# Optimization experiments

Hardware: AMD Instinct MI355X
Metric: run time of the kernel (lower is better)

The kernel has to match this reference:

```python
import jax, jax.numpy as jnp
import numpy as np

N_VIS, N_ASSOC, N_MOTOR, IN_DIM, T = 8192, 4096, 1024, 4096, 16
TAU_MEM, V_TH, TAU_ELIG = 20.0, 1.0, 500.0


def setup_inputs() -> dict:
    key = jax.random.key(0)
    ks = jax.random.split(key, 8)
    visual_input = jax.random.uniform(ks[0], (T, IN_DIM), dtype=jnp.float32)
    noise = jax.random.uniform(ks[1], (T, N_VIS), dtype=jnp.float32)  # replaces torch.rand_like
    dopamine = jax.random.normal(ks[2], (T,), dtype=jnp.float32)
    # visual_encoder: nn.Linear(4096, n_visual) default init (kaiming-uniform-ish); use small uniform
    lim = 1.0 / np.sqrt(IN_DIM)
    W_enc = jax.random.uniform(ks[3], (N_VIS, IN_DIM), minval=-lim, maxval=lim, dtype=jnp.float32)
    b_enc = jax.random.uniform(ks[4], (N_VIS,), minval=-lim, maxval=lim, dtype=jnp.float32)
    # v_to_a / a_to_m: uniform_(0.01, 0.05), no bias
    W_va = jax.random.uniform(ks[5], (N_ASSOC, N_VIS), minval=0.01, maxval=0.05, dtype=jnp.float32)
    W_am = jax.random.uniform(ks[6], (N_MOTOR, N_ASSOC), minval=0.01, maxval=0.05, dtype=jnp.float32)
    return {"visual_input": visual_input, "noise": noise, "dopamine": dopamine,
            "W_enc": W_enc, "b_enc": b_enc, "W_va": W_va, "W_am": W_am}


def reference(visual_input, noise, dopamine, W_enc, b_enc, W_va, W_am):
    decay_m = 1.0 - 1.0 / TAU_MEM
    decay_e = 1.0 - 1.0 / TAU_ELIG
    f32 = jnp.float32

    def step(carry, xs):
        vV, vA, vM, eVA, eAM, Wva, Wam = carry
        x, u, d = xs
        # visual encoding + Bernoulli spikes
        rates = jax.nn.sigmoid(x @ W_enc.T + b_enc)             # [n_visual]
        in_spk = (u < rates * 0.3).astype(f32)
        # LIF: visual layer
        vV = vV * decay_m + in_spk
        v_spk = (vV > V_TH).astype(f32)
        vV = vV * (1.0 - v_spk)
        # LIF: assoc layer
        vA = vA * decay_m + (v_spk @ Wva.T) * 0.1
        a_spk = (vA > V_TH).astype(f32)
        vA = vA * (1.0 - a_spk)
        # LIF: motor layer
        vM = vM * decay_m + (a_spk @ Wam.T) * 0.1
        m_spk = (vM > V_TH).astype(f32)
        vM = vM * (1.0 - m_spk)
        # DA-STDP eligibility traces (rank-1 updates)
        eVA = eVA * decay_e + jnp.outer(v_spk, a_spk) * 0.01    # [n_visual, n_assoc]
        eAM = eAM * decay_e + jnp.outer(a_spk, m_spk) * 0.01    # [n_assoc, n_motor]
        # conditional dopamine-gated weight update
        gate = jnp.abs(d) > 0.1
        Wva_new = jnp.clip(Wva + jnp.clip(d * eVA.T * 0.1, -0.01, 0.01), 0.0, 1.0)
        Wam_new = jnp.clip(Wam + jnp.clip(d * eAM.T * 0.1, -0.01, 0.01), 0.0, 1.0)
        Wva = jnp.where(gate, Wva_new, Wva)
        Wam = jnp.where(gate, Wam_new, Wam)
        eVA = jnp.where(gate, eVA * 0.5, eVA)
        eAM = jnp.where(gate, eAM * 0.5, eAM)
        return (vV, vA, vM, eVA, eAM, Wva, Wam), m_spk

    init = (jnp.zeros(N_VIS, f32), jnp.zeros(N_ASSOC, f32), jnp.zeros(N_MOTOR, f32),
            jnp.zeros((N_VIS, N_ASSOC), f32), jnp.zeros((N_ASSOC, N_MOTOR), f32),
            W_va, W_am)
    _, motor_spikes = jax.lax.scan(step, init, (visual_input, noise, dopamine))
    return motor_spikes  # [T, n_motor]
```

## Files before the change

### kernel.cpp

```cpp
#include <hip/hip_runtime.h>
#include <cstdint>

#define N_VIS   8192
#define N_ASSOC 4096
#define N_MOTOR 1024
#define IN_DIM  4096
#define T_STEPS 16

__global__ __launch_bounds__(256, 4) void encoder_kernel(
        const float* __restrict__ x, const float* __restrict__ noise,
        const float* __restrict__ W, const float* __restrict__ b,
        unsigned* __restrict__ vmask) {
    __shared__ float4 xs[16 * 64];
    const int tid = threadIdx.x;
    const int wave = tid >> 6, lane = tid & 63;
    const int r0 = blockIdx.x * 8 + wave * 2;
    const float4* W0 = (const float4*)(W + (size_t)r0 * IN_DIM);
    const float4* W1 = (const float4*)(W + (size_t)(r0 + 1) * IN_DIM);

    float a0[T_STEPS], a1[T_STEPS];
#pragma unroll
    for (int t = 0; t < T_STEPS; ++t) { a0[t] = 0.f; a1[t] = 0.f; }

    for (int c = 0; c < 16; ++c) {
        __syncthreads();
#pragma unroll
        for (int p = 0; p < 4; ++p) {
            int f = tid + p * 256;
            int t = f >> 6, c4 = f & 63;
            xs[f] = ((const float4*)(x + (size_t)t * IN_DIM + c * 256))[c4];
        }
        __syncthreads();
        float4 w0 = W0[c * 64 + lane];
        float4 w1 = W1[c * 64 + lane];
#pragma unroll
        for (int t = 0; t < T_STEPS; ++t) {
            float4 xv = xs[t * 64 + lane];
            a0[t] += w0.x*xv.x + w0.y*xv.y + w0.z*xv.z + w0.w*xv.w;
            a1[t] += w1.x*xv.x + w1.y*xv.y + w1.z*xv.z + w1.w*xv.w;
        }
    }
#pragma unroll
    for (int t = 0; t < T_STEPS; ++t) {
        float v;
        v = a0[t]; for (int o = 32; o; o >>= 1) v += __shfl_xor(v, o, 64); a0[t] = v;
        v = a1[t]; for (int o = 32; o; o >>= 1) v += __shfl_xor(v, o, 64); a1[t] = v;
    }
    if (lane == 0) {
        auto do_row = [&](int i, const float (&a)[T_STEPS]) {
            float bb = b[i];
            float v = 0.f;
            unsigned msk = 0;
#pragma unroll
            for (int t = 0; t < T_STEPS; ++t) {
                float logit = a[t] + bb;
                float rate = 1.0f / (1.0f + expf(-logit));
                float u = noise[t * N_VIS + i];
                float ins = (u < rate * 0.3f) ? 1.0f : 0.0f;
                v = v * 0.95f + ins;
                if (v > 1.0f) { msk |= (1u << t); v = 0.f; }
            }
            vmask[i] = msk;
        };
        do_row(r0, a0);
        do_row(r0 + 1, a1);
    }
}

__global__ void ktab_kernel(const float* __restrict__ dop, float* __restrict__ K) {
    __shared__ float C[256];
    __shared__ float sd[16];
    __shared__ unsigned sg[16];
    const int p = threadIdx.x;
    if (p < 16) {
        float d = dop[p];
        sd[p] = d;
        sg[p] = (fabsf(d) > 0.1f) ? 1u : 0u;
    }
    __syncthreads();
    {
        const int s = p >> 4, r = p & 15;
        float c = 0.f;
        if (s >= r) {
            c = 1.f;
            for (int u = r; u < s; ++u) {
                if (sg[u]) c *= 0.5f;
                c *= 0.998f;
            }
        }
        C[p] = c;
    }
    __syncthreads();
    {
        const int t = p >> 4, r = p & 15;
        float kk = 0.f;
        for (int s = r; s < t; ++s)
            if (sg[s]) kk += ((sd[s] * 0.1f) * 0.01f) * C[s * 16 + r];
        K[p] = kk;
    }
}

__global__ void ovl_kernel(const unsigned* __restrict__ mask, int words_per_block,
                           int* __restrict__ ovl) {
    const int p = threadIdx.x;
    const int r = p >> 4, t = p & 15;
    const unsigned* w = mask + blockIdx.x * words_per_block;
    int c = 0;
    for (int i = 0; i < words_per_block; ++i)
        c += (int)((w[i] >> r) & (w[i] >> t) & 1u);
    atomicAdd(&ovl[p], c);
}

template<int NC>
__global__ __launch_bounds__(256) void base_kernel(
        const float* __restrict__ W0, const unsigned* __restrict__ colmask,
        float* __restrict__ base) {
    const int j0 = blockIdx.x * 2;
    const int tid = threadIdx.x;
    const int lane = tid & 63, wv = tid >> 6;
    __shared__ float sred[4][32];

    const float4* Wr0 = (const float4*)(W0 + (size_t)j0 * (NC * 1024));
    const float4* Wr1 = (const float4*)(W0 + (size_t)(j0 + 1) * (NC * 1024));
    const uint4*  cm  = (const uint4*)colmask;

    float acc0[T_STEPS], acc1[T_STEPS];
#pragma unroll
    for (int t = 0; t < T_STEPS; ++t) { acc0[t] = 0.f; acc1[t] = 0.f; }

    for (int k = 0; k < NC; ++k) {
        float4 q0 = Wr0[tid + k * 256];
        float4 q1 = Wr1[tid + k * 256];
        uint4  m  = cm [tid + k * 256];
        unsigned plo = m.x | (m.y << 16);
        unsigned phi = m.z | (m.w << 16);
#pragma unroll
        for (int t = 0; t < T_STEPS; ++t) {
            float bx = (float)((plo >> t)        & 1u);
            float by = (float)((plo >> (t + 16)) & 1u);
            float bz = (float)((phi >> t)        & 1u);
            float bw = (float)((phi >> (t + 16)) & 1u);
            acc0[t] = fmaf(q0.x, bx, acc0[t]); acc0[t] = fmaf(q0.y, by, acc0[t]);
            acc0[t] = fmaf(q0.z, bz, acc0[t]); acc0[t] = fmaf(q0.w, bw, acc0[t]);
            acc1[t] = fmaf(q1.x, bx, acc1[t]); acc1[t] = fmaf(q1.y, by, acc1[t]);
            acc1[t] = fmaf(q1.z, bz, acc1[t]); acc1[t] = fmaf(q1.w, bw, acc1[t]);
        }
    }
#pragma unroll
    for (int t = 0; t < T_STEPS; ++t) {
        for (int o = 32; o; o >>= 1) acc0[t] += __shfl_down(acc0[t], o, 64);
        for (int o = 32; o; o >>= 1) acc1[t] += __shfl_down(acc1[t], o, 64);
    }
    if (lane == 0) {
#pragma unroll
        for (int t = 0; t < T_STEPS; ++t) {
            sred[wv][t]      = acc0[t];
            sred[wv][16 + t] = acc1[t];
        }
    }
    __syncthreads();
    if (tid < 32) {
        const int r = tid >> 4, t = tid & 15;
        float v = sred[0][tid] + sred[1][tid] + sred[2][tid] + sred[3][tid];
        base[(size_t)(j0 + r) * 16 + t] = v;
    }
}

__global__ __launch_bounds__(64) void rec_kernel(
        const float* __restrict__ base, const int* __restrict__ ovl,
        const float* __restrict__ K, unsigned* __restrict__ mask_out,
        float* __restrict__ outp, int out_stride) {
    __shared__ float KO[256];
    const int tid = threadIdx.x;
    for (int p = tid; p < 256; p += 64) {
        const int t = p >> 4, r = p & 15;
        KO[p] = K[p] * (float)ovl[r * 16 + t];
    }
    __syncthreads();

    const int j = blockIdx.x * 64 + tid;
    float br[T_STEPS];
#pragma unroll
    for (int t = 0; t < T_STEPS; ++t) br[t] = base[(size_t)j * 16 + t];

    float vmem = 0.f;
    unsigned am = 0;
#pragma unroll
    for (int t = 0; t < T_STEPS; ++t) {
        float I = br[t];
        for (int r = 0; r < t; ++r)
            if ((am >> r) & 1u) I += KO[t * 16 + r];
        vmem = vmem * 0.95f + I * 0.1f;
        const bool s = vmem > 1.0f;
        if (s) { vmem = 0.f; am |= (1u << t); }
        if (outp) outp[t * out_stride + j] = s ? 1.0f : 0.0f;
    }
    mask_out[j] = am;
}

extern "C" void kernel_launch(void* const* d_in, const int* in_sizes, int n_in,
                              void* d_out, int out_size, void* d_ws, size_t ws_size,
                              hipStream_t stream) {
    const float* x     = (const float*)d_in[0];
    const float* noise = (const float*)d_in[1];
    const float* dop   = (const float*)d_in[2];
    const float* W_enc = (const float*)d_in[3];
    const float* b_enc = (const float*)d_in[4];
    const float* W_va  = (const float*)d_in[5];
    const float* W_am  = (const float*)d_in[6];
    float* out = (float*)d_out;
    (void)in_sizes; (void)n_in; (void)out_size; (void)ws_size;

    char* ws = (char*)d_ws;
    size_t off = 0;
    unsigned* vmask  = (unsigned*)(ws + off); off += N_VIS * 4;
    unsigned* amask  = (unsigned*)(ws + off); off += N_ASSOC * 4;
    unsigned* mmask  = (unsigned*)(ws + off); off += N_MOTOR * 4;
    float*    K      = (float*)(ws + off);    off += 256 * 4;
    int*      ovl_v  = (int*)(ws + off);      off += 256 * 4;
    int*      ovl_a  = (int*)(ws + off);      off += 256 * 4;
    float*    baseVA = (float*)(ws + off);    off += (size_t)N_ASSOC * 16 * 4;
    float*    baseAM = (float*)(ws + off);    off += (size_t)N_MOTOR * 16 * 4;

    hipMemsetAsync(ovl_v, 0, 2 * 256 * 4, stream);

    ktab_kernel<<<1, 256, 0, stream>>>(dop, K);
    encoder_kernel<<<N_VIS / 8, 256, 0, stream>>>(x, noise, W_enc, b_enc, vmask);
    ovl_kernel<<<32, 256, 0, stream>>>(vmask, N_VIS / 32, ovl_v);
    base_kernel<8><<<N_ASSOC / 2, 256, 0, stream>>>(W_va, vmask, baseVA);
    rec_kernel<<<N_ASSOC / 64, 64, 0, stream>>>(baseVA, ovl_v, K, amask, nullptr, 0);
    ovl_kernel<<<16, 256, 0, stream>>>(amask, N_ASSOC / 16, ovl_a);
    base_kernel<4><<<N_MOTOR / 2, 256, 0, stream>>>(W_am, amask, baseAM);
    rec_kernel<<<N_MOTOR / 64, 64, 0, stream>>>(baseAM, ovl_a, K, mmask, out, N_MOTOR);
}
```

Before: 158.0 us.

## Double-buffer encoder input tiles and assign one row per wave in encoder and base kernels

```diff
diff --git a/kernel.cpp b/kernel.cpp
--- a/kernel.cpp
+++ b/kernel.cpp
@@ -7,63 +7,67 @@
 #define IN_DIM  4096
 #define T_STEPS 16
 
-__global__ __launch_bounds__(256, 4) void encoder_kernel(
+__global__ __launch_bounds__(512, 8) void encoder_kernel(
         const float* __restrict__ x, const float* __restrict__ noise,
         const float* __restrict__ W, const float* __restrict__ b,
         unsigned* __restrict__ vmask) {
-    __shared__ float4 xs[16 * 64];
+    __shared__ float4 xs[2][16 * 64];
     const int tid = threadIdx.x;
     const int wave = tid >> 6, lane = tid & 63;
-    const int r0 = blockIdx.x * 8 + wave * 2;
-    const float4* W0 = (const float4*)(W + (size_t)r0 * IN_DIM);
-    const float4* W1 = (const float4*)(W + (size_t)(r0 + 1) * IN_DIM);
-
-    float a0[T_STEPS], a1[T_STEPS];
-#pragma unroll
-    for (int t = 0; t < T_STEPS; ++t) { a0[t] = 0.f; a1[t] = 0.f; }
-
+    const int r = blockIdx.x * 8 + wave;
+    const float4* Wr = (const float4*)(W + (size_t)r * IN_DIM);
+
+    float a[T_STEPS];
+#pragma unroll
+    for (int t = 0; t < T_STEPS; ++t) a[t] = 0.f;
+
+    auto stage = [&](int c, int buf) {
+#pragma unroll
+        for (int p = 0; p < 2; ++p) {
+            int f = tid + p * 512;
+            int t = f >> 6, c4 = f & 63;
+            xs[buf][f] = ((const float4*)(x + (size_t)t * IN_DIM + c * 256))[c4];
+        }
+    };
+    stage(0, 0);
+    float4 wv = Wr[lane];
+    __syncthreads();
+
+#pragma unroll 1
     for (int c = 0; c < 16; ++c) {
+        const int cb = c & 1;
+        if (c < 15) stage(c + 1, cb ^ 1);
+        float4 nwv = wv;
+        if (c < 15) nwv = Wr[(c + 1) * 64 + lane];
+#pragma unroll
+        for (int t = 0; t < T_STEPS; ++t) {
+            float4 xv = xs[cb][t * 64 + lane];
+            a[t] += wv.x*xv.x + wv.y*xv.y + wv.z*xv.z + wv.w*xv.w;
+        }
         __syncthreads();
-#pragma unroll
-        for (int p = 0; p < 4; ++p) {
-            int f = tid + p * 256;
-            int t = f >> 6, c4 = f & 63;
-            xs[f] = ((const float4*)(x + (size_t)t * IN_DIM + c * 256))[c4];
-        }
-        __syncthreads();
-        float4 w0 = W0[c * 64 + lane];
-        float4 w1 = W1[c * 64 + lane];
+        wv = nwv;
+    }
+
+#pragma unroll
+    for (int t = 0; t < T_STEPS; ++t) {
+        float v = a[t];
+        for (int o = 32; o; o >>= 1) v += __shfl_xor(v, o, 64);
+        a[t] = v;
+    }
+    if (lane == 0) {
+        float bb = b[r];
+        float v = 0.f;
+        unsigned msk = 0;
 #pragma unroll
         for (int t = 0; t < T_STEPS; ++t) {
-            float4 xv = xs[t * 64 + lane];
-            a0[t] += w0.x*xv.x + w0.y*xv.y + w0.z*xv.z + w0.w*xv.w;
-            a1[t] += w1.x*xv.x + w1.y*xv.y + w1.z*xv.z + w1.w*xv.w;
-        }
-    }
-#pragma unroll
-    for (int t = 0; t < T_STEPS; ++t) {
-        float v;
-        v = a0[t]; for (int o = 32; o; o >>= 1) v += __shfl_xor(v, o, 64); a0[t] = v;
-        v = a1[t]; for (int o = 32; o; o >>= 1) v += __shfl_xor(v, o, 64); a1[t] = v;
-    }
-    if (lane == 0) {
-        auto do_row = [&](int i, const float (&a)[T_STEPS]) {
-            float bb = b[i];
-            float v = 0.f;
-            unsigned msk = 0;
-#pragma unroll
-            for (int t = 0; t < T_STEPS; ++t) {
-                float logit = a[t] + bb;
-                float rate = 1.0f / (1.0f + expf(-logit));
-                float u = noise[t * N_VIS + i];
-                float ins = (u < rate * 0.3f) ? 1.0f : 0.0f;
-                v = v * 0.95f + ins;
-                if (v > 1.0f) { msk |= (1u << t); v = 0.f; }
-            }
-            vmask[i] = msk;
-        };
-        do_row(r0, a0);
-        do_row(r0 + 1, a1);
+            float logit = a[t] + bb;
+            float rate = 1.0f / (1.0f + expf(-logit));
+            float u = noise[t * N_VIS + r];
+            float ins = (u < rate * 0.3f) ? 1.0f : 0.0f;
+            v = v * 0.95f + ins;
+            if (v > 1.0f) { msk |= (1u << t); v = 0.f; }
+        }
+        vmask[r] = msk;
     }
 }
 
@@ -112,57 +116,46 @@
 }
 
 template<int NC>
-__global__ __launch_bounds__(256) void base_kernel(
+__global__ __launch_bounds__(256, 8) void base_kernel(
         const float* __restrict__ W0, const unsigned* __restrict__ colmask,
         float* __restrict__ base) {
-    const int j0 = blockIdx.x * 2;
+    const int j = blockIdx.x;
     const int tid = threadIdx.x;
     const int lane = tid & 63, wv = tid >> 6;
-    __shared__ float sred[4][32];
-
-    const float4* Wr0 = (const float4*)(W0 + (size_t)j0 * (NC * 1024));
-    const float4* Wr1 = (const float4*)(W0 + (size_t)(j0 + 1) * (NC * 1024));
-    const uint4*  cm  = (const uint4*)colmask;
-
-    float acc0[T_STEPS], acc1[T_STEPS];
-#pragma unroll
-    for (int t = 0; t < T_STEPS; ++t) { acc0[t] = 0.f; acc1[t] = 0.f; }
-
+    __shared__ float sred[4][T_STEPS];
+
+    const float4* Wr = (const float4*)(W0 + (size_t)j * (NC * 1024));
+    const uint4*  cm = (const uint4*)colmask;
+
+    float acc[T_STEPS];
+#pragma unroll
+    for (int t = 0; t < T_STEPS; ++t) acc[t] = 0.f;
+
+#pragma unroll
     for (int k = 0; k < NC; ++k) {
-        float4 q0 = Wr0[tid + k * 256];
-        float4 q1 = Wr1[tid + k * 256];
-        uint4  m  = cm [tid + k * 256];
+        float4 q = Wr[tid + k * 256];
+        uint4  m = cm [tid + k * 256];
         unsigned plo = m.x | (m.y << 16);
         unsigned phi = m.z | (m.w << 16);
 #pragma unroll
         for (int t = 0; t < T_STEPS; ++t) {
-            float bx = (float)((plo >> t)        & 1u);
-            float by = (float)((plo >> (t + 16)) & 1u);
-            float bz = (float)((phi >> t)        & 1u);
-            float bw = (float)((phi >> (t + 16)) & 1u);
-            acc0[t] = fmaf(q0.x, bx, acc0[t]); acc0[t] = fmaf(q0.y, by, acc0[t]);
-            acc0[t] = fmaf(q0.z, bz, acc0[t]); acc0[t] = fmaf(q0.w, bw, acc0[t]);
-            acc1[t] = fmaf(q1.x, bx, acc1[t]); acc1[t] = fmaf(q1.y, by, acc1[t]);
-            acc1[t] = fmaf(q1.z, bz, acc1[t]); acc1[t] = fmaf(q1.w, bw, acc1[t]);
-        }
-    }
-#pragma unroll
-    for (int t = 0; t < T_STEPS; ++t) {
-        for (int o = 32; o; o >>= 1) acc0[t] += __shfl_down(acc0[t], o, 64);
-        for (int o = 32; o; o >>= 1) acc1[t] += __shfl_down(acc1[t], o, 64);
-    }
+            acc[t] = fmaf(q.x, (float)((plo >> t)        & 1u), acc[t]);
+            acc[t] = fmaf(q.y, (float)((plo >> (t + 16)) & 1u), acc[t]);
+            acc[t] = fmaf(q.z, (float)((phi >> t)        & 1u), acc[t]);
+            acc[t] = fmaf(q.w, (float)((phi >> (t + 16)) & 1u), acc[t]);
+        }
+    }
+#pragma unroll
+    for (int t = 0; t < T_STEPS; ++t)
+        for (int o = 32; o; o >>= 1) acc[t] += __shfl_down(acc[t], o, 64);
     if (lane == 0) {
 #pragma unroll
-        for (int t = 0; t < T_STEPS; ++t) {
-            sred[wv][t]      = acc0[t];
-            sred[wv][16 + t] = acc1[t];
-        }
-    }
-    __syncthreads();
-    if (tid < 32) {
-        const int r = tid >> 4, t = tid & 15;
+        for (int t = 0; t < T_STEPS; ++t) sred[wv][t] = acc[t];
+    }
+    __syncthreads();
+    if (tid < T_STEPS) {
         float v = sred[0][tid] + sred[1][tid] + sred[2][tid] + sred[3][tid];
-        base[(size_t)(j0 + r) * 16 + t] = v;
+        base[(size_t)j * 16 + tid] = v;
     }
 }
 
@@ -225,11 +218,11 @@
     hipMemsetAsync(ovl_v, 0, 2 * 256 * 4, stream);
 
     ktab_kernel<<<1, 256, 0, stream>>>(dop, K);
-    encoder_kernel<<<N_VIS / 8, 256, 0, stream>>>(x, noise, W_enc, b_enc, vmask);
+    encoder_kernel<<<N_VIS / 8, 512, 0, stream>>>(x, noise, W_enc, b_enc, vmask);
     ovl_kernel<<<32, 256, 0, stream>>>(vmask, N_VIS / 32, ovl_v);
-    base_kernel<8><<<N_ASSOC / 2, 256, 0, stream>>>(W_va, vmask, baseVA);
+    base_kernel<8><<<N_ASSOC, 256, 0, stream>>>(W_va, vmask, baseVA);
     rec_kernel<<<N_ASSOC / 64, 64, 0, stream>>>(baseVA, ovl_v, K, amask, nullptr, 0);
     ovl_kernel<<<16, 256, 0, stream>>>(amask, N_ASSOC / 16, ovl_a);
-    base_kernel<4><<<N_MOTOR / 2, 256, 0, stream>>>(W_am, amask, baseAM);
+    base_kernel<4><<<N_MOTOR, 256, 0, stream>>>(W_am, amask, baseAM);
     rec_kernel<<<N_MOTOR / 64, 64, 0, stream>>>(baseAM, ovl_a, K, mmask, out, N_MOTOR);
 }
```

Measured after the change: 187.3 us. 1.19x slower.
